# Kernel tuning notes

Hardware: AMD Instinct MI355X
Metric: run time of the kernel (lower is better)

The kernel has to match this reference:

```python
import jax, jax.numpy as jnp
import numpy as np

N, D, DEG, DEPTH, H = 50000, 300, 6, 3, 4
E = N * DEG
DK = D // H


def setup_inputs() -> dict:
    key = jax.random.key(0)
    ks = jax.random.split(key, 14)
    # circulant molecular-like graph: node i <-> i+k (k=1,2,3), edges emitted in
    # reverse pairs (2t, 2t+1) as required by reverse_edge()
    u = np.arange(N)
    src_l, dst_l = [], []
    for k in (1, 2, 3):
        v = (u + k) % N
        src_l.append(np.stack([u, v], 1).reshape(-1))
        dst_l.append(np.stack([v, u], 1).reshape(-1))
    src = np.concatenate(src_l).astype(np.int32)
    dst = np.concatenate(dst_l).astype(np.int32)
    # incoming-edge ids per node (every node has exactly DEG in-edges)
    order = np.argsort(dst, kind='stable')
    nbr_eids = order.reshape(N, DEG).astype(np.int32)
    nbr_mask = np.ones((N, DEG), dtype=bool)
    sd = 1.0 / np.sqrt(D)
    p = lambda i, shape: jax.random.normal(ks[i], shape, jnp.float32) * sd
    return {
        'f': jax.random.normal(ks[0], (N, D), jnp.float32),
        'x': jax.random.normal(ks[1], (E, D), jnp.float32),
        'Wq': p(2, (D, D)), 'bq': jnp.zeros((D,), jnp.float32),
        'Wk': p(3, (D, D)), 'bk': jnp.zeros((D,), jnp.float32),
        'Wv': p(4, (D, D)), 'bv': jnp.zeros((D,), jnp.float32),
        'Wo': p(5, (D, D)), 'bo': jnp.zeros((D,), jnp.float32),
        'W_mp': p(6, (DEPTH - 1, D, D)), 'b_mp': jnp.zeros((DEPTH - 1, D), jnp.float32),
        'W_last': p(7, (3 * D, D)), 'b_last': jnp.zeros((D,), jnp.float32),
        'src': jnp.asarray(src), 'dst': jnp.asarray(dst),
        'nbr_eids': jnp.asarray(nbr_eids), 'nbr_mask': jnp.asarray(nbr_mask),
    }


def reference(f, x, Wq, bq, Wk, bk, Wv, bv, Wo, bo, W_mp, b_mp, W_last, b_last,
              src, dst, nbr_eids, nbr_mask):
    n = f.shape[0]
    e = x.shape[0]
    rev = jnp.arange(e) ^ 1                     # reverse-pair permutation
    has_in = nbr_mask.any(axis=-1)              # [N]
    scale = 1.0 / jnp.sqrt(jnp.float32(DK))
    h = x                                       # edge state 'h' init from 'x'
    f_h = f                                     # node state 'f_h' init from 'f'
    for i in range(DEPTH - 1):
        # ragged mailbox of incoming edge states, padded to DEG
        m = jnp.where(nbr_mask[..., None], h[nbr_eids], 0.0)        # [N,DEG,D]
        q = (f_h @ Wq + bq).reshape(n, H, DK)                        # query = node feat
        k = (m @ Wk + bk).reshape(n, DEG, H, DK)                     # key   = mailbox
        v = ((m + f_h[:, None, :]) @ Wv + bv).reshape(n, DEG, H, DK) # value = mailbox + feat
        scores = jnp.einsum('nhk,ndhk->nhd', q, k) * scale          # [N,H,DEG]
        scores = jnp.where(nbr_mask[:, None, :], scores, -1e9)
        attn = jax.nn.softmax(scores, axis=-1)
        out = jnp.einsum('nhd,ndhk->nhk', attn, v).reshape(n, D) @ Wo + bo
        f_h = jnp.where(has_in[:, None], out, f_h)
        # edge update: m = f_h[src] - rev_h; h = relu(x + Linear_i(m))
        m_e = f_h[src] - h[rev]
        h = jax.nn.relu(x + m_e @ W_mp[i] + b_mp[i])
    # GEANet is undefined in the provided source -> identity pass-through
    mail = jax.ops.segment_sum(h, dst, num_segments=n)              # sum of in-edge states
    f_new = jnp.concatenate([mail, f_h, f], axis=-1) @ W_last + b_last
    f_final = jnp.where(has_in[:, None], f_new, f_h)
    return f_final, h
```

## Files before the change

### kernel.cpp

```cpp
#include <hip/hip_runtime.h>
#include <hip/hip_bf16.h>

typedef unsigned long long ull;
typedef unsigned int u32;
typedef unsigned short u16;
typedef __hip_bfloat16 bf16;
typedef __attribute__((ext_vector_type(8))) short v8s;
typedef __attribute__((ext_vector_type(4))) float v4f;
typedef __attribute__((ext_vector_type(2))) ull v2u;

#define NN 50000
#define DD 300
#define PD 320
#define EE (NN*6)

__device__ __forceinline__ u16 f2bf(float f) {
    u32 u = __float_as_uint(f);
    u32 r = u + 0x7FFFu + ((u >> 16) & 1u);
    return (u16)(r >> 16);
}
__device__ __forceinline__ u32 cvtpk(float lo, float hi) {
    u32 r;
    asm("v_cvt_pk_bf16_f32 %0, %1, %2" : "=v"(r) : "v"(lo), "v"(hi));
    return r;
}
__device__ __forceinline__ float lo16(u32 u) { return __uint_as_float(u << 16); }
__device__ __forceinline__ float hi16(u32 u) { return __uint_as_float(u & 0xffff0000u); }

__device__ __forceinline__ void gl16(const void* g, void* l) {
    __builtin_amdgcn_global_load_lds(
        (const __attribute__((address_space(1))) u32*)g,
        (__attribute__((address_space(3))) u32*)l, 16, 0, 0);
}

enum { E_BIAS = 0, E_MPF = 1 };
enum { O_F32 = 1, O_BF16 = 2 };

template<int EPI, int OUTM, int NSEG>
__global__ __launch_bounds__(512, 4)
void gemm_mfma(const bf16* __restrict__ A0, const bf16* __restrict__ A1,
               const bf16* __restrict__ A2, const bf16* __restrict__ A3,
               const bf16* __restrict__ A4,
               const int* __restrict__ srcidx, const bf16* __restrict__ FHW,
               const bf16* __restrict__ BT, const float* __restrict__ bias0,
               const bf16* __restrict__ xepi,
               float* __restrict__ Cf, bf16* __restrict__ Cb0,
               int M, long ycb)
{
    __shared__ __align__(16) char Als[64 * 640];
    const int tid = threadIdx.x;
    const int wave = tid >> 6, lane = tid & 63;
    const int l15 = lane & 15, l4 = lane >> 4;
    const int wr = wave >> 2, wc = wave & 3;
    const int rowBase = blockIdx.x * 64;
    const int gy = blockIdx.y;
    BT += (long)gy * 102400;
    if (bias0) bias0 += (long)gy * 320;
    if (Cb0) Cb0 += (long)gy * ycb;

    v4f acc[2][5];
    const v4f vzero = {0.f, 0.f, 0.f, 0.f};
    #pragma unroll
    for (int mt = 0; mt < 2; ++mt)
        #pragma unroll
        for (int nt = 0; nt < 5; ++nt) acc[mt][nt] = vzero;

    for (int seg = 0; seg < NSEG; ++seg) {
        const bf16* As = (seg == 0) ? A0 : (seg == 1 ? A1 : (seg == 2 ? A2 :
                         (seg == 3 ? A3 : A4)));
        if (seg) __syncthreads();
        #pragma unroll
        for (int s = 0; s < 5; ++s) {
            int c = tid + 512 * s;
            int r = c / 40, ch = c - r * 40;
            int grow = rowBase + r;
            grow = (grow < M) ? grow : (M - 1);
            int chs = ch ^ (r & 7);
            gl16(As + (long)grow * PD + chs * 8,
                 Als + (wave * 64 + 512 * s) * 16);
        }
        __syncthreads();

        const bf16* BTs = BT + (long)seg * 102400;
        #pragma unroll
        for (int ks = 0; ks < 10; ++ks) {
            v8s af[2];
            #pragma unroll
            for (int mt = 0; mt < 2; ++mt) {
                int rowL = wr * 32 + mt * 16 + l15;
                af[mt] = *(const v8s*)(Als +
                    ((rowL * 640 + ks * 64 + l4 * 16) ^ ((rowL & 7) << 4)));
            }
            #pragma unroll
            for (int nt = 0; nt < 5; ++nt) {
                int col = wc * 80 + nt * 16 + l15;
                v8s bfr = *(const v8s*)(BTs + (long)col * PD + ks * 32 + l4 * 8);
                #pragma unroll
                for (int mt = 0; mt < 2; ++mt)
                    acc[mt][nt] = __builtin_amdgcn_mfma_f32_16x16x32_bf16(
                        af[mt], bfr, acc[mt][nt], 0, 0, 0);
            }
        }
    }

    __syncthreads();
    #pragma unroll
    for (int nt = 0; nt < 5; ++nt) {
        int col = wc * 80 + nt * 16 + l15;
        float bvv = bias0 ? bias0[col] : 0.f;
        #pragma unroll
        for (int mt = 0; mt < 2; ++mt) {
            #pragma unroll
            for (int rr = 0; rr < 4; ++rr) {
                int rowL = wr * 32 + mt * 16 + l4 * 4 + rr;
                *(u16*)(Als + ((rowL * 640 + col * 2) ^ (((rowL >> 2) & 7) << 4)))
                    = f2bf(acc[mt][nt][rr] + bvv);
            }
        }
    }
    __syncthreads();

    #pragma unroll
    for (int s = 0; s < 5; ++s) {
        int c = tid + 512 * s;
        int r = c / 40, ch = c - r * 40;
        int grow = rowBase + r;
        if (grow >= M) continue;
        if (EPI == E_MPF) {
            v2u hv = *(const v2u*)(Als +
                (((r ^ 1) * 640 + ch * 16) ^ (((r >> 2) & 7) << 4)));
            v2u xv = *(const v2u*)(xepi + (long)grow * PD + ch * 8);
            int sr = srcidx[grow];
            v2u fw = *(const v2u*)(FHW + (long)sr * PD + ch * 8);
            float vf[8];
            #pragma unroll
            for (int w = 0; w < 2; ++w) {
                u32 h0 = (u32)hv[w], h1 = (u32)(hv[w] >> 32);
                u32 x0 = (u32)xv[w], x1 = (u32)(xv[w] >> 32);
                u32 f0 = (u32)fw[w], f1 = (u32)(fw[w] >> 32);
                vf[w*4+0] = fmaxf(lo16(x0) + lo16(f0) - lo16(h0), 0.f);
                vf[w*4+1] = fmaxf(hi16(x0) + hi16(f0) - hi16(h0), 0.f);
                vf[w*4+2] = fmaxf(lo16(x1) + lo16(f1) - lo16(h1), 0.f);
                vf[w*4+3] = fmaxf(hi16(x1) + hi16(f1) - hi16(h1), 0.f);
            }
            if (OUTM & O_BF16) {
                v2u rv;
                rv[0] = (ull)cvtpk(vf[0], vf[1]) | ((ull)cvtpk(vf[2], vf[3]) << 32);
                rv[1] = (ull)cvtpk(vf[4], vf[5]) | ((ull)cvtpk(vf[6], vf[7]) << 32);
                *(v2u*)(Cb0 + (long)grow * PD + ch * 8) = rv;
            }
            if (OUTM & O_F32) {
                int col0 = ch * 8;
                if (col0 < DD) {
                    float4 lo = {vf[0], vf[1], vf[2], vf[3]};
                    *(float4*)(Cf + (long)grow * DD + col0) = lo;
                    if (col0 + 4 < DD) {
                        float4 hi4 = {vf[4], vf[5], vf[6], vf[7]};
                        *(float4*)(Cf + (long)grow * DD + col0 + 4) = hi4;
                    }
                }
            }
        } else {
            v2u val = *(const v2u*)(Als + ((c * 16) ^ (((r >> 2) & 7) << 4)));
            if (OUTM & O_BF16)
                *(v2u*)(Cb0 + (long)grow * PD + ch * 8) = val;
            if (OUTM & O_F32) {
                int col0 = ch * 8;
                if (col0 < DD) {
                    u32 a0 = (u32)val[0], a1 = (u32)(val[0] >> 32);
                    float4 lo = {lo16(a0), hi16(a0), lo16(a1), hi16(a1)};
                    *(float4*)(Cf + (long)grow * DD + col0) = lo;
                    if (col0 + 4 < DD) {
                        u32 b0 = (u32)val[1], b1 = (u32)(val[1] >> 32);
                        float4 hi4 = {lo16(b0), hi16(b0), lo16(b1), hi16(b1)};
                        *(float4*)(Cf + (long)grow * DD + col0 + 4) = hi4;
                    }
                }
            }
        }
    }
}

__global__ __launch_bounds__(256)
void scoreU_k(const bf16* __restrict__ G0, const bf16* __restrict__ G1,
              const bf16* __restrict__ G2, const bf16* __restrict__ G3,
              const bf16* __restrict__ h, const int* __restrict__ nbr,
              bf16* __restrict__ U0, bf16* __restrict__ U1,
              bf16* __restrict__ U2, bf16* __restrict__ U3)
{
    int wave = threadIdx.x >> 6, lane = threadIdx.x & 63;
    int n = blockIdx.x * 4 + wave;
    if (n >= NN) return;
    int eid[6];
    #pragma unroll
    for (int d = 0; d < 6; ++d) eid[d] = nbr[n * 6 + d];

    bool act = lane < 40;
    int cl = act ? lane : 0;
    long go = (long)n * PD + cl * 8;

    float g[4][8];
    #pragma unroll
    for (int hh = 0; hh < 4; ++hh) {
        const bf16* Gp = (hh == 0) ? G0 : (hh == 1) ? G1 : (hh == 2) ? G2 : G3;
        v2u gv = *(const v2u*)(Gp + go);
        u32 w0 = (u32)gv[0], w1 = (u32)(gv[0] >> 32);
        u32 w2 = (u32)gv[1], w3 = (u32)(gv[1] >> 32);
        g[hh][0] = lo16(w0); g[hh][1] = hi16(w0);
        g[hh][2] = lo16(w1); g[hh][3] = hi16(w1);
        g[hh][4] = lo16(w2); g[hh][5] = hi16(w2);
        g[hh][6] = lo16(w3); g[hh][7] = hi16(w3);
        if (!act)
            #pragma unroll
            for (int i = 0; i < 8; ++i) g[hh][i] = 0.f;
    }
    v2u hp[6];
    #pragma unroll
    for (int d = 0; d < 6; ++d)
        hp[d] = *(const v2u*)(h + (long)eid[d] * PD + cl * 8);

    float s0[6], s1[6], s2[6], s3[6];
    #pragma unroll
    for (int d = 0; d < 6; ++d) {
        u32 w0 = (u32)hp[d][0], w1 = (u32)(hp[d][0] >> 32);
        u32 w2 = (u32)hp[d][1], w3 = (u32)(hp[d][1] >> 32);
        float hf[8] = {lo16(w0), hi16(w0), lo16(w1), hi16(w1),
                       lo16(w2), hi16(w2), lo16(w3), hi16(w3)};
        float p0 = 0, p1 = 0, p2 = 0, p3 = 0;
        #pragma unroll
        for (int i = 0; i < 8; ++i) {
            p0 += g[0][i] * hf[i];
            p1 += g[1][i] * hf[i];
            p2 += g[2][i] * hf[i];
            p3 += g[3][i] * hf[i];
        }
        #pragma unroll
        for (int off = 32; off; off >>= 1) {
            p0 += __shfl_xor(p0, off);
            p1 += __shfl_xor(p1, off);
            p2 += __shfl_xor(p2, off);
            p3 += __shfl_xor(p3, off);
        }
        s0[d] = p0; s1[d] = p1; s2[d] = p2; s3[d] = p3;
    }

    const float scale = 0.1154700538379252f;
    float at[4][6];
    {
        float m0 = -1e30f, m1 = -1e30f, m2 = -1e30f, m3 = -1e30f;
        #pragma unroll
        for (int d = 0; d < 6; ++d) {
            s0[d] *= scale; s1[d] *= scale; s2[d] *= scale; s3[d] *= scale;
            m0 = fmaxf(m0, s0[d]); m1 = fmaxf(m1, s1[d]);
            m2 = fmaxf(m2, s2[d]); m3 = fmaxf(m3, s3[d]);
        }
        float t0 = 0, t1 = 0, t2 = 0, t3 = 0;
        #pragma unroll
        for (int d = 0; d < 6; ++d) {
            at[0][d] = expf(s0[d] - m0); t0 += at[0][d];
            at[1][d] = expf(s1[d] - m1); t1 += at[1][d];
            at[2][d] = expf(s2[d] - m2); t2 += at[2][d];
            at[3][d] = expf(s3[d] - m3); t3 += at[3][d];
        }
        t0 = 1.f / t0; t1 = 1.f / t1; t2 = 1.f / t2; t3 = 1.f / t3;
        #pragma unroll
        for (int d = 0; d < 6; ++d) {
            at[0][d] *= t0; at[1][d] *= t1; at[2][d] *= t2; at[3][d] *= t3;
        }
    }

    float u[4][8];
    #pragma unroll
    for (int hh = 0; hh < 4; ++hh)
        #pragma unroll
        for (int i = 0; i < 8; ++i) u[hh][i] = 0.f;
    #pragma unroll
    for (int d = 0; d < 6; ++d) {
        u32 w0 = (u32)hp[d][0], w1 = (u32)(hp[d][0] >> 32);
        u32 w2 = (u32)hp[d][1], w3 = (u32)(hp[d][1] >> 32);
        float hf[8] = {lo16(w0), hi16(w0), lo16(w1), hi16(w1),
                       lo16(w2), hi16(w2), lo16(w3), hi16(w3)};
        #pragma unroll
        for (int i = 0; i < 8; ++i) {
            u[0][i] += at[0][d] * hf[i];
            u[1][i] += at[1][d] * hf[i];
            u[2][i] += at[2][d] * hf[i];
            u[3][i] += at[3][d] * hf[i];
        }
    }
    if (act) {
        #pragma unroll
        for (int hh = 0; hh < 4; ++hh) {
            bf16* Up = (hh == 0) ? U0 : (hh == 1) ? U1 : (hh == 2) ? U2 : U3;
            v2u r;
            r[0] = (ull)cvtpk(u[hh][0], u[hh][1]) |
                   ((ull)cvtpk(u[hh][2], u[hh][3]) << 32);
            r[1] = (ull)cvtpk(u[hh][4], u[hh][5]) |
                   ((ull)cvtpk(u[hh][6], u[hh][7]) << 32);
            *(v2u*)(Up + go) = r;
        }
    }
}

__global__ __launch_bounds__(256)
void mailf_k(const float* __restrict__ h, const int* __restrict__ nbr,
             bf16* __restrict__ mail)
{
    int idx = blockIdx.x * 256 + threadIdx.x;
    if (idx >= NN * 80) return;
    int n = idx / 80, c4 = idx - n * 80;
    float4 s = {0.f, 0.f, 0.f, 0.f};
    if (c4 < 75) {
        const int* e = nbr + n * 6;
        #pragma unroll
        for (int d = 0; d < 6; ++d) {
            float4 v = *(const float4*)(h + (long)e[d] * DD + c4 * 4);
            s.x += v.x; s.y += v.y; s.z += v.z; s.w += v.w;
        }
    }
    ull r = (ull)cvtpk(s.x, s.y) | ((ull)cvtpk(s.z, s.w) << 32);
    *(ull*)(mail + (long)n * PD + c4 * 4) = r;
}

__global__ __launch_bounds__(256)
void conv_k(const float* __restrict__ in, bf16* __restrict__ out, int rows)
{
    long idx = (long)blockIdx.x * 256 + threadIdx.x;
    if (idx >= (long)rows * 40) return;
    int r = (int)(idx / 40), ch = (int)(idx - (long)r * 40);
    int c4 = ch * 2;
    float4 a = {0, 0, 0, 0}, b = {0, 0, 0, 0};
    if (c4 < 75)     a = *(const float4*)(in + (long)r * DD + c4 * 4);
    if (c4 + 1 < 75) b = *(const float4*)(in + (long)r * DD + c4 * 4 + 4);
    v2u v;
    v[0] = (ull)cvtpk(a.x, a.y) | ((ull)cvtpk(a.z, a.w) << 32);
    v[1] = (ull)cvtpk(b.x, b.y) | ((ull)cvtpk(b.z, b.w) << 32);
    *(v2u*)(out + (long)r * PD + ch * 8) = v;
}

__global__ __launch_bounds__(256)
void tw_k(const float* __restrict__ W, bf16* __restrict__ BT)
{
    int idx = blockIdx.x * 256 + threadIdx.x;
    if (idx >= 320 * 320) return;
    int nn = idx / 320, kk = idx - nn * 320;
    u16 v = 0;
    if (nn < DD && kk < DD) v = f2bf(W[kk * DD + nn]);
    ((u16*)BT)[idx] = v;
}

__global__ __launch_bounds__(256)
void twf_k(const float* __restrict__ W, float* __restrict__ WT)
{
    __shared__ float t[32][33];
    int bx = blockIdx.x % 10, by = blockIdx.x / 10;
    int r0 = by * 32, c0 = bx * 32;
    int tx = threadIdx.x & 31, ty = threadIdx.x >> 5;
    #pragma unroll
    for (int i = 0; i < 4; ++i) {
        int r = r0 + ty + i * 8, c = c0 + tx;
        t[ty + i * 8][tx] = (r < DD && c < DD) ? W[r * DD + c] : 0.f;
    }
    __syncthreads();
    #pragma unroll
    for (int i = 0; i < 4; ++i)
        WT[(c0 + ty + i * 8) * 320 + r0 + tx] = t[tx][ty + i * 8];
}

__global__ __launch_bounds__(256)
void wqk_k(const float* __restrict__ WqT, const float* __restrict__ Wk,
           bf16* __restrict__ slab)
{
    int idx = blockIdx.x * 256 + threadIdx.x;
    if (idx >= 1280 * 320) return;
    int c = idx / 320, k = idx - c * 320;
    int hh = c / 320;
    int ci = c - hh * 320;
    float v = 0.f;
    if (ci < DD && k < DD) {
        int jb = hh * 75;
        for (int j = 0; j < 75; ++j)
            v += WqT[(jb + j) * 320 + k] * Wk[ci * DD + jb + j];
    }
    ((u16*)slab)[idx] = f2bf(v);
}

__global__ __launch_bounds__(256)
void wcomp_k(const float* __restrict__ WvT, const float* __restrict__ Wo,
             bf16* __restrict__ slab)
{
    int idx = blockIdx.x * 256 + threadIdx.x;
    if (idx >= 5 * 320 * 320) return;
    int s = idx / 102400, rem = idx - s * 102400;
    int c = rem / 320, k = rem - c * 320;
    float v = 0.f;
    if (c < DD && k < DD) {
        int jb = (s < 4) ? s * 75 : 0;
        int jn = (s < 4) ? 75 : 300;
        for (int j = 0; j < jn; ++j)
            v += WvT[(jb + j) * 320 + k] * Wo[(jb + j) * DD + c];
    }
    ((u16*)slab)[idx] = f2bf(v);
}

__global__ void bias_k(const float* __restrict__ WkT, const float* __restrict__ Wo,
                       const float* __restrict__ bq, const float* __restrict__ bv,
                       const float* __restrict__ bo, const float* __restrict__ bmp,
                       const float* __restrict__ blast, float* __restrict__ outb)
{
    int a = blockIdx.x, i = threadIdx.x;
    float v = 0.f;
    if (i < DD) {
        if (a < 4) {
            for (int j = 0; j < 75; ++j)
                v += bq[a * 75 + j] * WkT[(a * 75 + j) * 320 + i];
        } else if (a == 4) {
            for (int j = 0; j < DD; ++j) v += bv[j] * Wo[j * DD + i];
            v += bo[i];
        } else if (a == 5) v = bmp[i];
        else if (a == 6) v = bmp[DD + i];
        else v = blast[i];
    }
    outb[a * 320 + i] = v;
}

extern "C" void kernel_launch(void* const* d_in, const int* in_sizes, int n_in,
                              void* d_out, int out_size, void* d_ws, size_t ws_size,
                              hipStream_t stream)
{
    const float* f     = (const float*)d_in[0];
    const float* x     = (const float*)d_in[1];
    const float* Wq    = (const float*)d_in[2];
    const float* bq    = (const float*)d_in[3];
    const float* Wk    = (const float*)d_in[4];
    const float* bv    = (const float*)d_in[7];
    const float* Wv    = (const float*)d_in[6];
    const float* Wo    = (const float*)d_in[8];
    const float* bo    = (const float*)d_in[9];
    const float* Wmp   = (const float*)d_in[10];
    const float* bmp   = (const float*)d_in[11];
    const float* Wlast = (const float*)d_in[12];
    const float* blast = (const float*)d_in[13];
    const int*   src   = (const int*)d_in[14];
    const int*   nbr   = (const int*)d_in[16];

    float* out     = (float*)d_out;
    float* f_final = out;
    float* h_final = out + (long)NN * DD;

    char* ws = (char*)d_ws;
    bf16* xb  = (bf16*)(ws);
    bf16* h1b = (bf16*)(ws + 192000000LL);
    bf16* fb  = (bf16*)(ws + 576000000LL);
    bf16* G0  = (bf16*)(ws + 608000000LL);
    bf16* G1  = (bf16*)(ws + 640000000LL);
    bf16* G2  = (bf16*)(ws + 672000000LL);
    bf16* G3  = (bf16*)(ws + 704000000LL);
    bf16* FHb = (bf16*)(ws + 736000000LL);
    bf16* WT  = (bf16*)(ws + 768000000LL);
    float* BIAS = (float*)(ws + 771300000LL);
    float* WqT  = (float*)(ws + 771400000LL);
    float* WkT  = (float*)(ws + 771850000LL);
    float* WvT  = (float*)(ws + 772300000LL);
    auto slot = [&](int i) { return WT + (long)i * 320 * 320; };
    bf16* qk   = slot(0);
    bf16* fh5  = slot(4);
    float* g0p = BIAS;
    float* b2p = BIAS + 1280;
    float* bm0p = BIAS + 1600;  float* bm1p = BIAS + 1920;
    float* blp = BIAS + 2240;
    bf16* MLb = G0;
    bf16* FHW = G1;

    dim3 blk(256), blk5(512);
    const int gN = (NN + 63) / 64;
    const int gE = (EE + 63) / 64;

    conv_k<<<(int)(((long)EE * 40 + 255) / 256), blk, 0, stream>>>(x, xb, EE);
    conv_k<<<(int)(((long)NN * 40 + 255) / 256), blk, 0, stream>>>(f, fb, NN);
    twf_k<<<100, blk, 0, stream>>>(Wq, WqT);
    twf_k<<<100, blk, 0, stream>>>(Wk, WkT);
    twf_k<<<100, blk, 0, stream>>>(Wv, WvT);
    wqk_k<<<1600, blk, 0, stream>>>(WqT, Wk, qk);
    wcomp_k<<<2000, blk, 0, stream>>>(WvT, Wo, fh5);
    tw_k<<<400, blk, 0, stream>>>(Wmp, slot(9));
    tw_k<<<400, blk, 0, stream>>>(Wmp + 90000, slot(10));
    tw_k<<<400, blk, 0, stream>>>(Wlast, slot(11));
    tw_k<<<400, blk, 0, stream>>>(Wlast + 90000, slot(12));
    tw_k<<<400, blk, 0, stream>>>(Wlast + 180000, slot(13));
    bias_k<<<8, 320, 0, stream>>>(WkT, Wo, bq, bv, bo, bmp, blast, BIAS);

    for (int it = 0; it < 2; ++it) {
        const bf16* hb  = it ? h1b : xb;
        const bf16* fhb = it ? FHb : fb;
        const bf16* mpW = it ? slot(10) : slot(9);
        const float* bmP = it ? bm1p : bm0p;
        gemm_mfma<E_BIAS, O_BF16, 1><<<dim3(gN, 4), blk5, 0, stream>>>(
            fhb, nullptr, nullptr, nullptr, nullptr, nullptr, nullptr,
            qk, g0p, nullptr, nullptr, G0, NN, 16000000);
        scoreU_k<<<(NN + 3) / 4, blk, 0, stream>>>(G0, G1, G2, G3, hb, nbr,
                                                   G0, G1, G2, G3);
        gemm_mfma<E_BIAS, O_BF16, 5><<<gN, blk5, 0, stream>>>(
            G0, G1, G2, G3, fhb, nullptr, nullptr, fh5, b2p, nullptr,
            nullptr, FHb, NN, 0);
        gemm_mfma<E_BIAS, O_BF16, 1><<<gN, blk5, 0, stream>>>(
            FHb, nullptr, nullptr, nullptr, nullptr, nullptr, nullptr,
            mpW, bmP, nullptr, nullptr, FHW, NN, 0);
        if (it == 0) {
            gemm_mfma<E_MPF, O_BF16, 1><<<gE, blk5, 0, stream>>>(
                hb, nullptr, nullptr, nullptr, nullptr, src, FHW,
                mpW, nullptr, xb, nullptr, h1b, EE, 0);
        } else {
            gemm_mfma<E_MPF, O_F32, 1><<<gE, blk5, 0, stream>>>(
                hb, nullptr, nullptr, nullptr, nullptr, src, FHW,
                mpW, nullptr, xb, h_final, nullptr, EE, 0);
        }
    }

    mailf_k<<<(NN * 80 + 255) / 256, blk, 0, stream>>>(h_final, nbr, MLb);
    gemm_mfma<E_BIAS, O_F32, 3><<<gN, blk5, 0, stream>>>(
        MLb, FHb, fb, nullptr, nullptr, nullptr, nullptr, slot(11), blp,
        nullptr, f_final, nullptr, NN, 0);
}
```

Measured before the change: 2.263 ms.

## Double-buffer A tiles and process two row tiles per GEMM block

```diff
diff --git a/kernel.cpp b/kernel.cpp
--- a/kernel.cpp
+++ b/kernel.cpp
@@ -36,7 +36,7 @@
 enum { E_BIAS = 0, E_MPF = 1 };
 enum { O_F32 = 1, O_BF16 = 2 };
 
-template<int EPI, int OUTM, int NSEG>
+template<int EPI, int OUTM, int NSEG, int TPB>
 __global__ __launch_bounds__(512, 4)
 void gemm_mfma(const bf16* __restrict__ A0, const bf16* __restrict__ A1,
                const bf16* __restrict__ A2, const bf16* __restrict__ A3,
@@ -47,12 +47,14 @@
                float* __restrict__ Cf, bf16* __restrict__ Cb0,
                int M, long ycb)
 {
-    __shared__ __align__(16) char Als[64 * 640];
+    constexpr int U = NSEG * TPB;
+    constexpr int NBUF = (U > 1) ? 2 : 1;
+    __shared__ __align__(16) char Als[NBUF][64 * 640];
     const int tid = threadIdx.x;
     const int wave = tid >> 6, lane = tid & 63;
     const int l15 = lane & 15, l4 = lane >> 4;
     const int wr = wave >> 2, wc = wave & 3;
-    const int rowBase = blockIdx.x * 64;
+    const int rowBase0 = blockIdx.x * (64 * TPB);
     const int gy = blockIdx.y;
     BT += (long)gy * 102400;
     if (bias0) bias0 += (long)gy * 320;
@@ -65,22 +67,34 @@
         #pragma unroll
         for (int nt = 0; nt < 5; ++nt) acc[mt][nt] = vzero;
 
-    for (int seg = 0; seg < NSEG; ++seg) {
-        const bf16* As = (seg == 0) ? A0 : (seg == 1 ? A1 : (seg == 2 ? A2 :
-                         (seg == 3 ? A3 : A4)));
-        if (seg) __syncthreads();
+    auto APTR = [&](int seg) -> const bf16* {
+        return (seg == 0) ? A0 : (seg == 1 ? A1 : (seg == 2 ? A2 :
+               (seg == 3 ? A3 : A4)));
+    };
+    auto stage = [&](int u, char* buf) {
+        int seg = u % NSEG, tile = u / NSEG;
+        const bf16* As = APTR(seg);
+        int rb = rowBase0 + tile * 64;
         #pragma unroll
         for (int s = 0; s < 5; ++s) {
             int c = tid + 512 * s;
             int r = c / 40, ch = c - r * 40;
-            int grow = rowBase + r;
+            int grow = rb + r;
             grow = (grow < M) ? grow : (M - 1);
             int chs = ch ^ (r & 7);
             gl16(As + (long)grow * PD + chs * 8,
-                 Als + (wave * 64 + 512 * s) * 16);
-        }
-        __syncthreads();
-
+                 buf + (wave * 64 + 512 * s) * 16);
+        }
+    };
+
+    stage(0, Als[0]);
+    __syncthreads();
+
+    for (int u = 0; u < U; ++u) {
+        char* cur = Als[(NBUF == 2) ? (u & 1) : 0];
+        if (u + 1 < U) stage(u + 1, Als[(NBUF == 2) ? ((u + 1) & 1) : 0]);
+
+        const int seg = u % NSEG;
         const bf16* BTs = BT + (long)seg * 102400;
         #pragma unroll
         for (int ks = 0; ks < 10; ++ks) {
@@ -88,7 +102,7 @@
             #pragma unroll
             for (int mt = 0; mt < 2; ++mt) {
                 int rowL = wr * 32 + mt * 16 + l15;
-                af[mt] = *(const v8s*)(Als +
+                af[mt] = *(const v8s*)(cur +
                     ((rowL * 640 + ks * 64 + l4 * 16) ^ ((rowL & 7) << 4)));
             }
             #pragma unroll
@@ -101,82 +115,95 @@
                         af[mt], bfr, acc[mt][nt], 0, 0, 0);
             }
         }
-    }
-
-    __syncthreads();
-    #pragma unroll
-    for (int nt = 0; nt < 5; ++nt) {
-        int col = wc * 80 + nt * 16 + l15;
-        float bvv = bias0 ? bias0[col] : 0.f;
-        #pragma unroll
-        for (int mt = 0; mt < 2; ++mt) {
+        __syncthreads();
+
+        if (seg == NSEG - 1) {
+            const int tile = u / NSEG;
+            const int rb = rowBase0 + tile * 64;
             #pragma unroll
-            for (int rr = 0; rr < 4; ++rr) {
-                int rowL = wr * 32 + mt * 16 + l4 * 4 + rr;
-                *(u16*)(Als + ((rowL * 640 + col * 2) ^ (((rowL >> 2) & 7) << 4)))
-                    = f2bf(acc[mt][nt][rr] + bvv);
-            }
-        }
-    }
-    __syncthreads();
-
-    #pragma unroll
-    for (int s = 0; s < 5; ++s) {
-        int c = tid + 512 * s;
-        int r = c / 40, ch = c - r * 40;
-        int grow = rowBase + r;
-        if (grow >= M) continue;
-        if (EPI == E_MPF) {
-            v2u hv = *(const v2u*)(Als +
-                (((r ^ 1) * 640 + ch * 16) ^ (((r >> 2) & 7) << 4)));
-            v2u xv = *(const v2u*)(xepi + (long)grow * PD + ch * 8);
-            int sr = srcidx[grow];
-            v2u fw = *(const v2u*)(FHW + (long)sr * PD + ch * 8);
-            float vf[8];
-            #pragma unroll
-            for (int w = 0; w < 2; ++w) {
-                u32 h0 = (u32)hv[w], h1 = (u32)(hv[w] >> 32);
-                u32 x0 = (u32)xv[w], x1 = (u32)(xv[w] >> 32);
-                u32 f0 = (u32)fw[w], f1 = (u32)(fw[w] >> 32);
-                vf[w*4+0] = fmaxf(lo16(x0) + lo16(f0) - lo16(h0), 0.f);
-                vf[w*4+1] = fmaxf(hi16(x0) + hi16(f0) - hi16(h0), 0.f);
-                vf[w*4+2] = fmaxf(lo16(x1) + lo16(f1) - lo16(h1), 0.f);
-                vf[w*4+3] = fmaxf(hi16(x1) + hi16(f1) - hi16(h1), 0.f);
-            }
-            if (OUTM & O_BF16) {
-                v2u rv;
-                rv[0] = (ull)cvtpk(vf[0], vf[1]) | ((ull)cvtpk(vf[2], vf[3]) << 32);
-                rv[1] = (ull)cvtpk(vf[4], vf[5]) | ((ull)cvtpk(vf[6], vf[7]) << 32);
-                *(v2u*)(Cb0 + (long)grow * PD + ch * 8) = rv;
-            }
-            if (OUTM & O_F32) {
-                int col0 = ch * 8;
-                if (col0 < DD) {
-                    float4 lo = {vf[0], vf[1], vf[2], vf[3]};
-                    *(float4*)(Cf + (long)grow * DD + col0) = lo;
-                    if (col0 + 4 < DD) {
-                        float4 hi4 = {vf[4], vf[5], vf[6], vf[7]};
-                        *(float4*)(Cf + (long)grow * DD + col0 + 4) = hi4;
+            for (int nt = 0; nt < 5; ++nt) {
+                int col = wc * 80 + nt * 16 + l15;
+                float bvv = bias0 ? bias0[col] : 0.f;
+                #pragma unroll
+                for (int mt = 0; mt < 2; ++mt) {
+                    #pragma unroll
+                    for (int rr = 0; rr < 4; ++rr) {
+                        int rowL = wr * 32 + mt * 16 + l4 * 4 + rr;
+                        *(u16*)(cur + ((rowL * 640 + col * 2) ^
+                                       (((rowL >> 2) & 7) << 4)))
+                            = f2bf(acc[mt][nt][rr] + bvv);
                     }
                 }
             }
-        } else {
-            v2u val = *(const v2u*)(Als + ((c * 16) ^ (((r >> 2) & 7) << 4)));
-            if (OUTM & O_BF16)
-                *(v2u*)(Cb0 + (long)grow * PD + ch * 8) = val;
-            if (OUTM & O_F32) {
-                int col0 = ch * 8;
-                if (col0 < DD) {
-                    u32 a0 = (u32)val[0], a1 = (u32)(val[0] >> 32);
-                    float4 lo = {lo16(a0), hi16(a0), lo16(a1), hi16(a1)};
-                    *(float4*)(Cf + (long)grow * DD + col0) = lo;
-                    if (col0 + 4 < DD) {
-                        u32 b0 = (u32)val[1], b1 = (u32)(val[1] >> 32);
-                        float4 hi4 = {lo16(b0), hi16(b0), lo16(b1), hi16(b1)};
-                        *(float4*)(Cf + (long)grow * DD + col0 + 4) = hi4;
+            __syncthreads();
+            #pragma unroll
+            for (int s = 0; s < 5; ++s) {
+                int c = tid + 512 * s;
+                int r = c / 40, ch = c - r * 40;
+                int grow = rb + r;
+                if (grow >= M) continue;
+                if (EPI == E_MPF) {
+                    v2u hv = *(const v2u*)(cur +
+                        (((r ^ 1) * 640 + ch * 16) ^ (((r >> 2) & 7) << 4)));
+                    v2u xv = *(const v2u*)(xepi + (long)grow * PD + ch * 8);
+                    int sr = srcidx[grow];
+                    v2u fw = *(const v2u*)(FHW + (long)sr * PD + ch * 8);
+                    float vf[8];
+                    #pragma unroll
+                    for (int w = 0; w < 2; ++w) {
+                        u32 h0 = (u32)hv[w], h1 = (u32)(hv[w] >> 32);
+                        u32 x0 = (u32)xv[w], x1 = (u32)(xv[w] >> 32);
+                        u32 f0 = (u32)fw[w], f1 = (u32)(fw[w] >> 32);
+                        vf[w*4+0] = fmaxf(lo16(x0) + lo16(f0) - lo16(h0), 0.f);
+                        vf[w*4+1] = fmaxf(hi16(x0) + hi16(f0) - hi16(h0), 0.f);
+                        vf[w*4+2] = fmaxf(lo16(x1) + lo16(f1) - lo16(h1), 0.f);
+                        vf[w*4+3] = fmaxf(hi16(x1) + hi16(f1) - hi16(h1), 0.f);
+                    }
+                    if (OUTM & O_BF16) {
+                        v2u rv;
+                        rv[0] = (ull)cvtpk(vf[0], vf[1]) |
+                                ((ull)cvtpk(vf[2], vf[3]) << 32);
+                        rv[1] = (ull)cvtpk(vf[4], vf[5]) |
+                                ((ull)cvtpk(vf[6], vf[7]) << 32);
+                        *(v2u*)(Cb0 + (long)grow * PD + ch * 8) = rv;
+                    }
+                    if (OUTM & O_F32) {
+                        int col0 = ch * 8;
+                        if (col0 < DD) {
+                            float4 lo = {vf[0], vf[1], vf[2], vf[3]};
+                            *(float4*)(Cf + (long)grow * DD + col0) = lo;
+                            if (col0 + 4 < DD) {
+                                float4 hi4 = {vf[4], vf[5], vf[6], vf[7]};
+                                *(float4*)(Cf + (long)grow * DD + col0 + 4) = hi4;
+                            }
+                        }
+                    }
+                } else {
+                    int lr = c * 16;
+                    v2u val = *(const v2u*)(cur + (lr ^ (((r >> 2) & 7) << 4)));
+                    if (OUTM & O_BF16)
+                        *(v2u*)(Cb0 + (long)grow * PD + ch * 8) = val;
+                    if (OUTM & O_F32) {
+                        int col0 = ch * 8;
+                        if (col0 < DD) {
+                            u32 a0 = (u32)val[0], a1 = (u32)(val[0] >> 32);
+                            float4 lo = {lo16(a0), hi16(a0), lo16(a1), hi16(a1)};
+                            *(float4*)(Cf + (long)grow * DD + col0) = lo;
+                            if (col0 + 4 < DD) {
+                                u32 b0 = (u32)val[1], b1 = (u32)(val[1] >> 32);
+                                float4 hi4 = {lo16(b0), hi16(b0),
+                                              lo16(b1), hi16(b1)};
+                                *(float4*)(Cf + (long)grow * DD + col0 + 4) = hi4;
+                            }
+                        }
                     }
                 }
             }
+            #pragma unroll
+            for (int mt = 0; mt < 2; ++mt)
+                #pragma unroll
+                for (int nt = 0; nt < 5; ++nt) acc[mt][nt] = vzero;
+            if (u + 2 < U) __syncthreads();
         }
     }
 }
@@ -473,8 +500,8 @@
     bf16* FHW = G1;
 
     dim3 blk(256), blk5(512);
-    const int gN = (NN + 63) / 64;
-    const int gE = (EE + 63) / 64;
+    const int gN2 = (NN + 127) / 128;
+    const int gE2 = (EE + 127) / 128;
 
     conv_k<<<(int)(((long)EE * 40 + 255) / 256), blk, 0, stream>>>(x, xb, EE);
     conv_k<<<(int)(((long)NN * 40 + 255) / 256), blk, 0, stream>>>(f, fb, NN);
@@ -495,30 +522,30 @@
         const bf16* fhb = it ? FHb : fb;
         const bf16* mpW = it ? slot(10) : slot(9);
         const float* bmP = it ? bm1p : bm0p;
-        gemm_mfma<E_BIAS, O_BF16, 1><<<dim3(gN, 4), blk5, 0, stream>>>(
+        gemm_mfma<E_BIAS, O_BF16, 1, 2><<<dim3(gN2, 4), blk5, 0, stream>>>(
             fhb, nullptr, nullptr, nullptr, nullptr, nullptr, nullptr,
             qk, g0p, nullptr, nullptr, G0, NN, 16000000);
         scoreU_k<<<(NN + 3) / 4, blk, 0, stream>>>(G0, G1, G2, G3, hb, nbr,
                                                    G0, G1, G2, G3);
-        gemm_mfma<E_BIAS, O_BF16, 5><<<gN, blk5, 0, stream>>>(
+        gemm_mfma<E_BIAS, O_BF16, 5, 2><<<gN2, blk5, 0, stream>>>(
             G0, G1, G2, G3, fhb, nullptr, nullptr, fh5, b2p, nullptr,
             nullptr, FHb, NN, 0);
-        gemm_mfma<E_BIAS, O_BF16, 1><<<gN, blk5, 0, stream>>>(
+        gemm_mfma<E_BIAS, O_BF16, 1, 2><<<gN2, blk5, 0, stream>>>(
             FHb, nullptr, nullptr, nullptr, nullptr, nullptr, nullptr,
             mpW, bmP, nullptr, nullptr, FHW, NN, 0);
         if (it == 0) {
-            gemm_mfma<E_MPF, O_BF16, 1><<<gE, blk5, 0, stream>>>(
+            gemm_mfma<E_MPF, O_BF16, 1, 2><<<gE2, blk5, 0, stream>>>(
                 hb, nullptr, nullptr, nullptr, nullptr, src, FHW,
                 mpW, nullptr, xb, nullptr, h1b, EE, 0);
         } else {
-            gemm_mfma<E_MPF, O_F32, 1><<<gE, blk5, 0, stream>>>(
+            gemm_mfma<E_MPF, O_F32, 1, 2><<<gE2, blk5, 0, stream>>>(
                 hb, nullptr, nullptr, nullptr, nullptr, src, FHW,
                 mpW, nullptr, xb, h_final, nullptr, EE, 0);
         }
     }
 
     mailf_k<<<(NN * 80 + 255) / 256, blk, 0, stream>>>(h_final, nbr, MLb);
-    gemm_mfma<E_BIAS, O_F32, 3><<<gN, blk5, 0, stream>>>(
+    gemm_mfma<E_BIAS, O_F32, 3, 2><<<gN2, blk5, 0, stream>>>(
         MLb, FHb, fb, nullptr, nullptr, nullptr, nullptr, slot(11), blp,
         nullptr, f_final, nullptr, NN, 0);
 }
```

After: 3.808 ms. +68.2%, slower.

## Gather f_h[src] minus reverse edge state in GEMM prologue instead of distributing

Applied to the files above, without the earlier changes.

```diff
diff --git a/kernel.cpp b/kernel.cpp
--- a/kernel.cpp
+++ b/kernel.cpp
@@ -27,13 +27,22 @@
 __device__ __forceinline__ float lo16(u32 u) { return __uint_as_float(u << 16); }
 __device__ __forceinline__ float hi16(u32 u) { return __uint_as_float(u & 0xffff0000u); }
 
+__device__ __forceinline__ u32 sub2bf(u32 a, u32 b) {
+    return cvtpk(lo16(a) - lo16(b), hi16(a) - hi16(b));
+}
+__device__ __forceinline__ ull sub4bf(ull a, ull b) {
+    u32 l = sub2bf((u32)a, (u32)b);
+    u32 h = sub2bf((u32)(a >> 32), (u32)(b >> 32));
+    return (ull)l | ((ull)h << 32);
+}
+
 __device__ __forceinline__ void gl16(const void* g, void* l) {
     __builtin_amdgcn_global_load_lds(
         (const __attribute__((address_space(1))) u32*)g,
         (__attribute__((address_space(3))) u32*)l, 16, 0, 0);
 }
 
-enum { E_BIAS = 0, E_MPF = 1 };
+enum { E_BIAS = 0, E_MPG = 1 };
 enum { O_F32 = 1, O_BF16 = 2 };
 
 template<int EPI, int OUTM, int NSEG>
@@ -41,7 +50,7 @@
 void gemm_mfma(const bf16* __restrict__ A0, const bf16* __restrict__ A1,
                const bf16* __restrict__ A2, const bf16* __restrict__ A3,
                const bf16* __restrict__ A4,
-               const int* __restrict__ srcidx, const bf16* __restrict__ FHW,
+               const int* __restrict__ srcidx,
                const bf16* __restrict__ BT, const float* __restrict__ bias0,
                const bf16* __restrict__ xepi,
                float* __restrict__ Cf, bf16* __restrict__ Cb0,
@@ -75,9 +84,19 @@
             int r = c / 40, ch = c - r * 40;
             int grow = rowBase + r;
             grow = (grow < M) ? grow : (M - 1);
-            int chs = ch ^ (r & 7);
-            gl16(As + (long)grow * PD + chs * 8,
-                 Als + (wave * 64 + 512 * s) * 16);
+            if (EPI == E_MPG) {
+                int sr = srcidx[grow];
+                v2u a = *(const v2u*)(A0 + (long)sr * PD + ch * 8);
+                v2u b = *(const v2u*)(A1 + (long)(grow ^ 1) * PD + ch * 8);
+                v2u v;
+                v[0] = sub4bf(a[0], b[0]);
+                v[1] = sub4bf(a[1], b[1]);
+                *(v2u*)(Als + ((c * 16) ^ ((r & 7) << 4))) = v;
+            } else {
+                int chs = ch ^ (r & 7);
+                gl16(As + (long)grow * PD + chs * 8,
+                     Als + (wave * 64 + 512 * s) * 16);
+            }
         }
         __syncthreads();
 
@@ -126,55 +145,32 @@
         int r = c / 40, ch = c - r * 40;
         int grow = rowBase + r;
         if (grow >= M) continue;
-        if (EPI == E_MPF) {
-            v2u hv = *(const v2u*)(Als +
-                (((r ^ 1) * 640 + ch * 16) ^ (((r >> 2) & 7) << 4)));
+        v2u val = *(const v2u*)(Als + ((c * 16) ^ (((r >> 2) & 7) << 4)));
+        if (EPI == E_MPG) {
             v2u xv = *(const v2u*)(xepi + (long)grow * PD + ch * 8);
-            int sr = srcidx[grow];
-            v2u fw = *(const v2u*)(FHW + (long)sr * PD + ch * 8);
-            float vf[8];
             #pragma unroll
             for (int w = 0; w < 2; ++w) {
-                u32 h0 = (u32)hv[w], h1 = (u32)(hv[w] >> 32);
-                u32 x0 = (u32)xv[w], x1 = (u32)(xv[w] >> 32);
-                u32 f0 = (u32)fw[w], f1 = (u32)(fw[w] >> 32);
-                vf[w*4+0] = fmaxf(lo16(x0) + lo16(f0) - lo16(h0), 0.f);
-                vf[w*4+1] = fmaxf(hi16(x0) + hi16(f0) - hi16(h0), 0.f);
-                vf[w*4+2] = fmaxf(lo16(x1) + lo16(f1) - lo16(h1), 0.f);
-                vf[w*4+3] = fmaxf(hi16(x1) + hi16(f1) - hi16(h1), 0.f);
+                u32 a0 = (u32)val[w], a1 = (u32)(val[w] >> 32);
+                u32 x0 = (u32)xv[w],  x1 = (u32)(xv[w] >> 32);
+                u32 r0 = cvtpk(fmaxf(lo16(a0) + lo16(x0), 0.f),
+                               fmaxf(hi16(a0) + hi16(x0), 0.f));
+                u32 r1 = cvtpk(fmaxf(lo16(a1) + lo16(x1), 0.f),
+                               fmaxf(hi16(a1) + hi16(x1), 0.f));
+                val[w] = (ull)r0 | ((ull)r1 << 32);
             }
-            if (OUTM & O_BF16) {
-                v2u rv;
-                rv[0] = (ull)cvtpk(vf[0], vf[1]) | ((ull)cvtpk(vf[2], vf[3]) << 32);
-                rv[1] = (ull)cvtpk(vf[4], vf[5]) | ((ull)cvtpk(vf[6], vf[7]) << 32);
-                *(v2u*)(Cb0 + (long)grow * PD + ch * 8) = rv;
-            }
-            if (OUTM & O_F32) {
-                int col0 = ch * 8;
-                if (col0 < DD) {
-                    float4 lo = {vf[0], vf[1], vf[2], vf[3]};
-                    *(float4*)(Cf + (long)grow * DD + col0) = lo;
-                    if (col0 + 4 < DD) {
-                        float4 hi4 = {vf[4], vf[5], vf[6], vf[7]};
-                        *(float4*)(Cf + (long)grow * DD + col0 + 4) = hi4;
-                    }
-                }
-            }
-        } else {
-            v2u val = *(const v2u*)(Als + ((c * 16) ^ (((r >> 2) & 7) << 4)));
-            if (OUTM & O_BF16)
-                *(v2u*)(Cb0 + (long)grow * PD + ch * 8) = val;
-            if (OUTM & O_F32) {
-                int col0 = ch * 8;
-                if (col0 < DD) {
-                    u32 a0 = (u32)val[0], a1 = (u32)(val[0] >> 32);
-                    float4 lo = {lo16(a0), hi16(a0), lo16(a1), hi16(a1)};
-                    *(float4*)(Cf + (long)grow * DD + col0) = lo;
-                    if (col0 + 4 < DD) {
-                        u32 b0 = (u32)val[1], b1 = (u32)(val[1] >> 32);
-                        float4 hi4 = {lo16(b0), hi16(b0), lo16(b1), hi16(b1)};
-                        *(float4*)(Cf + (long)grow * DD + col0 + 4) = hi4;
-                    }
+        }
+        if (OUTM & O_BF16)
+            *(v2u*)(Cb0 + (long)grow * PD + ch * 8) = val;
+        if (OUTM & O_F32) {
+            int col0 = ch * 8;
+            if (col0 < DD) {
+                u32 a0 = (u32)val[0], a1 = (u32)(val[0] >> 32);
+                float4 lo = {lo16(a0), hi16(a0), lo16(a1), hi16(a1)};
+                *(float4*)(Cf + (long)grow * DD + col0) = lo;
+                if (col0 + 4 < DD) {
+                    u32 b0 = (u32)val[1], b1 = (u32)(val[1] >> 32);
+                    float4 hi4 = {lo16(b0), hi16(b0), lo16(b1), hi16(b1)};
+                    *(float4*)(Cf + (long)grow * DD + col0 + 4) = hi4;
                 }
             }
         }
@@ -470,7 +466,6 @@
     float* bm0p = BIAS + 1600;  float* bm1p = BIAS + 1920;
     float* blp = BIAS + 2240;
     bf16* MLb = G0;
-    bf16* FHW = G1;
 
     dim3 blk(256), blk5(512);
     const int gN = (NN + 63) / 64;
@@ -496,29 +491,26 @@
         const bf16* mpW = it ? slot(10) : slot(9);
         const float* bmP = it ? bm1p : bm0p;
         gemm_mfma<E_BIAS, O_BF16, 1><<<dim3(gN, 4), blk5, 0, stream>>>(
-            fhb, nullptr, nullptr, nullptr, nullptr, nullptr, nullptr,
+            fhb, nullptr, nullptr, nullptr, nullptr, nullptr,
             qk, g0p, nullptr, nullptr, G0, NN, 16000000);
         scoreU_k<<<(NN + 3) / 4, blk, 0, stream>>>(G0, G1, G2, G3, hb, nbr,
                                                    G0, G1, G2, G3);
         gemm_mfma<E_BIAS, O_BF16, 5><<<gN, blk5, 0, stream>>>(
-            G0, G1, G2, G3, fhb, nullptr, nullptr, fh5, b2p, nullptr,
+            G0, G1, G2, G3, fhb, nullptr, fh5, b2p, nullptr,
             nullptr, FHb, NN, 0);
-        gemm_mfma<E_BIAS, O_BF16, 1><<<gN, blk5, 0, stream>>>(
-            FHb, nullptr, nullptr, nullptr, nullptr, nullptr, nullptr,
-            mpW, bmP, nullptr, nullptr, FHW, NN, 0);
         if (it == 0) {
-            gemm_mfma<E_MPF, O_BF16, 1><<<gE, blk5, 0, stream>>>(
-                hb, nullptr, nullptr, nullptr, nullptr, src, FHW,
-                mpW, nullptr, xb, nullptr, h1b, EE, 0);
+            gemm_mfma<E_MPG, O_BF16, 1><<<gE, blk5, 0, stream>>>(
+                FHb, hb, nullptr, nullptr, nullptr, src,
+                mpW, bm0p, xb, nullptr, h1b, EE, 0);
         } else {
-            gemm_mfma<E_MPF, O_F32, 1><<<gE, blk5, 0, stream>>>(
-                hb, nullptr, nullptr, nullptr, nullptr, src, FHW,
-                mpW, nullptr, xb, h_final, nullptr, EE, 0);
+            gemm_mfma<E_MPG, O_F32, 1><<<gE, blk5, 0, stream>>>(
+                FHb, hb, nullptr, nullptr, nullptr, src,
+                mpW, bm1p, xb, h_final, nullptr, EE, 0);
         }
     }
 
     mailf_k<<<(NN * 80 + 255) / 256, blk, 0, stream>>>(h_final, nbr, MLb);
     gemm_mfma<E_BIAS, O_F32, 3><<<gN, blk5, 0, stream>>>(
-        MLb, FHb, fb, nullptr, nullptr, nullptr, nullptr, slot(11), blp,
+        MLb, FHb, fb, nullptr, nullptr, nullptr, slot(11), blp,
         nullptr, f_final, nullptr, NN, 0);
 }
```

Result: faster. 2.176 ms (-3.9%).
